# Kernel optimization log

Measured on AMD Instinct MI355X. Metric: run time of the kernel, lower is better.

## Reference

```python
import jax, jax.numpy as jnp
import numpy as np

B, L, D, E, F, K = 2, 1024, 768, 16, 3072, 2


def setup_inputs() -> dict:
    key = jax.random.key(0)
    ks = jax.random.split(key, 6)
    s = 0.02  # GPT-style init scale
    x = jax.random.normal(ks[0], (B, L, D), dtype=jnp.float32)
    wr = jax.random.normal(ks[1], (E, D), dtype=jnp.float32) * s   # router.weight [out,in]
    w1 = jax.random.normal(ks[2], (E, F, D), dtype=jnp.float32) * s  # expert fc1 weights
    b1 = jnp.zeros((E, F), dtype=jnp.float32)
    w2 = jax.random.normal(ks[3], (E, D, F), dtype=jnp.float32) * s  # expert fc2 weights
    b2 = jnp.zeros((E, D), dtype=jnp.float32)
    return {"x": x, "wr": wr, "w1": w1, "b1": b1, "w2": w2, "b2": b2}


def reference(x, wr, w1, b1, w2, b2):
    # --- router: softmax over experts, top-k gate built by scatter ---
    logits = jnp.einsum("bld,ed->ble", x, wr)            # [B,L,E]
    probs = jax.nn.softmax(logits, axis=-1)
    top_p, ix = jax.lax.top_k(probs, K)                   # [B,L,K]
    # gate[b,l,e] = top_p where e in ix else 0  (scatter_ equivalent)
    gate = jnp.sum(jax.nn.one_hot(ix, E, dtype=x.dtype) * top_p[..., None], axis=-2)  # [B,L,E]
    # --- dense: every expert over every token (matches original loop) ---
    h = jnp.einsum("bld,efd->blef", x, w1) + b1           # [B,L,E,F]
    h = jax.nn.gelu(h, approximate=False)                 # torch nn.GELU (exact erf)
    y = jnp.einsum("blef,edf->bled", h, w2) + b2          # [B,L,E,D]
    out = x + jnp.einsum("bled,ble->bld", y, gate)        # gated combine + residual
    return out
```

## Files before the change

### kernel.cpp

```cpp
#include <hip/hip_runtime.h>


#define D_      768
#define E_      16
#define F_      3072
#define NTOK    2048
#define NROWS   4096
#define SEG     384
#define MAXROWS 6144
#define KLEN    768
#define NT      12
#define LDT     776

typedef __attribute__((ext_vector_type(4))) unsigned int   u32x4;
typedef __attribute__((ext_vector_type(8))) unsigned short u16x8;
typedef __attribute__((ext_vector_type(8))) short          v8bf;
typedef __attribute__((ext_vector_type(4))) float          f32x4;

static __device__ inline unsigned short f2bf(float f) {
    unsigned u = __builtin_bit_cast(unsigned, f);
    u += 0x7fffu + ((u >> 16) & 1u);
    return (unsigned short)(u >> 16);
}
static __device__ __forceinline__ unsigned cvt_pk_bf16(float lo, float hi) {
    unsigned r;
    asm("v_cvt_pk_bf16_f32 %0, %1, %2" : "=v"(r) : "v"(lo), "v"(hi));
    return r;
}

__global__ void router_kernel(const float* __restrict__ x, const float* __restrict__ wr,
                              int* __restrict__ idx, float* __restrict__ gate) {
    const int tok  = blockIdx.x;
    const int lane = threadIdx.x;
    const float* xr = x + (size_t)tok * D_;

    float xv[12];
#pragma unroll
    for (int j = 0; j < 12; ++j) xv[j] = xr[lane + 64 * j];

    float lg[E_];
#pragma unroll
    for (int e = 0; e < E_; ++e) {
        const float* w = wr + (size_t)e * D_;
        float acc = 0.f;
#pragma unroll
        for (int j = 0; j < 12; ++j) acc += xv[j] * w[lane + 64 * j];
#pragma unroll
        for (int s = 32; s > 0; s >>= 1) acc += __shfl_xor(acc, s, 64);
        lg[e] = acc;
    }

    float m = lg[0];
#pragma unroll
    for (int e = 1; e < E_; ++e) m = fmaxf(m, lg[e]);
    float p[E_], s = 0.f;
#pragma unroll
    for (int e = 0; e < E_; ++e) { p[e] = expf(lg[e] - m); s += p[e]; }
    const float inv = 1.f / s;

    int e0 = 0; float p0 = p[0];
#pragma unroll
    for (int e = 1; e < E_; ++e) if (p[e] > p0) { p0 = p[e]; e0 = e; }
    int e1 = -1; float p1 = -1.f;
#pragma unroll
    for (int e = 0; e < E_; ++e) if (e != e0 && p[e] > p1) { p1 = p[e]; e1 = e; }

    if (lane == 0) {
        idx[tok * 2 + 0] = e0;  gate[tok * 2 + 0] = p0 * inv;
        idx[tok * 2 + 1] = e1;  gate[tok * 2 + 1] = p1 * inv;
    }
}

__global__ void build_kernel(const int* __restrict__ idx, const float* __restrict__ gate,
                             int* __restrict__ rowmap, float* __restrict__ rowgate,
                             int* __restrict__ posOf, int* __restrict__ meta) {
    __shared__ int cur[E_];
    const int t = threadIdx.x;
    if (t < E_) cur[t] = 0;
    __syncthreads();
    for (int i = t; i < MAXROWS; i += 256) { rowmap[i] = 0; rowgate[i] = 0.f; }
    __syncthreads();
    for (int i = t; i < NROWS; i += 256) {
        const int e = idx[i];
        const int o = atomicAdd(&cur[e], 1);
        if (o < SEG) {
            const int pos = e * SEG + o;
            rowmap[pos]  = i >> 1;
            rowgate[pos] = gate[i];
            posOf[i]     = pos;
        } else {
            posOf[i] = e * SEG;
        }
    }
    __syncthreads();
    if (t < E_) meta[t] = cur[t] < SEG ? cur[t] : SEG;
}

__global__ void gather_kernel(const float* __restrict__ x, const int* __restrict__ rowmap,
                              unsigned short* __restrict__ Xg) {
    const int g = blockIdx.x * 256 + threadIdx.x;
    const int pos = g / (D_ / 8), c = g % (D_ / 8);
    const int tok = rowmap[pos];
    const float* src = x + (size_t)tok * D_ + c * 8;
    f32x4 a = *(const f32x4*)src;
    f32x4 b = *(const f32x4*)(src + 4);
    u16x8 o;
    o[0] = f2bf(a[0]); o[1] = f2bf(a[1]); o[2] = f2bf(a[2]); o[3] = f2bf(a[3]);
    o[4] = f2bf(b[0]); o[5] = f2bf(b[1]); o[6] = f2bf(b[2]); o[7] = f2bf(b[3]);
    *(u16x8*)(Xg + (size_t)pos * D_ + c * 8) = o;
}

template <int EPI, int NCBSH>
__global__ __launch_bounds__(512, 2)
void gemm_kernel(const unsigned short* __restrict__ Ag, const float* __restrict__ Bw,
                 const float* __restrict__ bias, unsigned short* __restrict__ C0,
                 unsigned short* __restrict__ C123, const float* __restrict__ rowgate,
                 const int* __restrict__ meta, const int K, const int N) {
    const int bid   = blockIdx.x;
    const int e     = bid & 15;
    const int rest  = bid >> 4;
    const int n     = rest & ((1 << NCBSH) - 1);
    const int split = rest >> NCBSH;
    const int m0    = e * SEG;
    const int n0    = n * 96;
    const int kOff  = split * KLEN;

    __shared__ unsigned short Bs[96 * LDT];

    const int t    = threadIdx.x;
    const int lane = t & 63;
    const int wv   = t >> 6;
    const int r16  = lane & 15;
    const int h    = lane >> 4;

    {
#pragma unroll
        for (int i = 0; i < 18; ++i) {
            const int p = t + 512 * i;
            const int row = p / 96, pc = p % 96;
            const float* src = Bw + ((size_t)e * N + n0 + row) * K + kOff + pc * 8;
            f32x4 lo = *(const f32x4*)src;
            f32x4 hi = *(const f32x4*)(src + 4);
            u32x4 q;
            q[0] = cvt_pk_bf16(lo[0], lo[1]);
            q[1] = cvt_pk_bf16(lo[2], lo[3]);
            q[2] = cvt_pk_bf16(hi[0], hi[1]);
            q[3] = cvt_pk_bf16(hi[2], hi[3]);
            *(u32x4*)&Bs[row * LDT + pc * 8] = q;
        }
    }
    __syncthreads();

    const int cnt = meta[e];
    if (wv * 48 >= cnt) return;

    f32x4 acc[3][6];
#pragma unroll
    for (int i = 0; i < 3; ++i)
#pragma unroll
        for (int j = 0; j < 6; ++j) acc[i][j] = (f32x4){0.f, 0.f, 0.f, 0.f};

    const unsigned short* aBase =
        Ag + (size_t)(m0 + wv * 48 + r16) * K + kOff + h * 8;

    u32x4 pa[6], pb[6];

    auto loadSet = [&](int kt, u32x4* dst) {
#pragma unroll
        for (int mf = 0; mf < 3; ++mf)
#pragma unroll
            for (int ks = 0; ks < 2; ++ks)
                dst[mf * 2 + ks] =
                    *(const u32x4*)(aBase + (size_t)(mf * 16) * K + kt * 64 + ks * 32);
    };
    auto step = [&](int kt, const u32x4* a) {
#pragma unroll
        for (int ks = 0; ks < 2; ++ks) {
            v8bf bfr[6];
#pragma unroll
            for (int nf = 0; nf < 6; ++nf)
                bfr[nf] = *(const v8bf*)&Bs[(nf * 16 + r16) * LDT + kt * 64 + ks * 32 + h * 8];
#pragma unroll
            for (int mf = 0; mf < 3; ++mf) {
                const v8bf af = __builtin_bit_cast(v8bf, a[mf * 2 + ks]);
#pragma unroll
                for (int nf = 0; nf < 6; ++nf)
                    acc[mf][nf] = __builtin_amdgcn_mfma_f32_16x16x32_bf16(
                        af, bfr[nf], acc[mf][nf], 0, 0, 0);
            }
        }
    };

    loadSet(0, pa);
    loadSet(1, pb);
#pragma unroll
    for (int kt = 0; kt < NT; kt += 2) {
        step(kt, pa);
        if (kt + 2 < NT) loadSet(kt + 2, pa);
        step(kt + 1, pb);
        if (kt + 3 < NT) loadSet(kt + 3, pb);
    }

    unsigned short* myC = (EPI == 0 || split == 0)
                        ? C0 : C123 + (size_t)(split - 1) * MAXROWS * N;
#pragma unroll
    for (int mf = 0; mf < 3; ++mf) {
#pragma unroll
        for (int jj = 0; jj < 4; ++jj) {
            const int rr = m0 + wv * 48 + mf * 16 + h * 4 + jj;
            float gt = 0.f;
            if (EPI == 1) gt = rowgate[rr];
#pragma unroll
            for (int nf = 0; nf < 6; ++nf) {
                const int cc = n0 + nf * 16 + r16;
                float v = acc[mf][nf][jj];
                if (EPI == 0) {
                    v += bias[e * N + cc];
                    const float ge = 0.5f * v * (1.f + erff(v * 0.70710678118654752f));
                    myC[(size_t)rr * N + cc] = f2bf(ge);
                } else {
                    if (split == 0) v += bias[e * N + cc];
                    myC[(size_t)rr * N + cc] = f2bf(v * gt);
                }
            }
        }
    }
}

__global__ void combine_kernel(const float* __restrict__ x,
                               const unsigned short* __restrict__ Yp0,
                               const unsigned short* __restrict__ Yp123,
                               const int* __restrict__ posOf, float* __restrict__ out,
                               const int nsplit) {
    const int tok = blockIdx.x;
    const int t   = threadIdx.x;
    const int p0 = posOf[tok * 2 + 0];
    const int p1 = posOf[tok * 2 + 1];
    f32x4 v = *(const f32x4*)(x + (size_t)tok * D_ + t * 4);
    for (int s = 0; s < nsplit; ++s) {
        const unsigned short* base = (s == 0) ? Yp0
                                   : Yp123 + (size_t)(s - 1) * MAXROWS * D_;
        const unsigned short* a = base + (size_t)p0 * D_ + t * 4;
        const unsigned short* b = base + (size_t)p1 * D_ + t * 4;
#pragma unroll
        for (int i = 0; i < 4; ++i) {
            v[i] += __builtin_bit_cast(float, (unsigned)a[i] << 16);
            v[i] += __builtin_bit_cast(float, (unsigned)b[i] << 16);
        }
    }
    *(f32x4*)(out + (size_t)tok * D_ + t * 4) = v;
}

extern "C" void kernel_launch(void* const* d_in, const int* in_sizes, int n_in,
                              void* d_out, int out_size, void* d_ws, size_t ws_size,
                              hipStream_t stream) {
    const float* x  = (const float*)d_in[0];
    const float* wr = (const float*)d_in[1];
    const float* w1 = (const float*)d_in[2];
    const float* b1 = (const float*)d_in[3];
    const float* w2 = (const float*)d_in[4];
    const float* b2 = (const float*)d_in[5];
    float* out = (float*)d_out;

    char* wsp = (char*)d_ws;
    int*            idxP    = (int*)(wsp + 0);
    float*          gateP   = (float*)(wsp + 16384);
    int*            posOf   = (int*)(wsp + 32768);
    int*            rowmap  = (int*)(wsp + 49152);
    float*          rowgate = (float*)(wsp + 73728);
    int*            meta    = (int*)(wsp + 98304);
    const size_t    XG_OFF  = 131072;
    const size_t    PLANE   = (size_t)MAXROWS * D_ * 2;
    const size_t    H_OFF   = XG_OFF + PLANE;
    const size_t    H_B     = (size_t)MAXROWS * F_ * 2;
    unsigned short* Xg    = (unsigned short*)(wsp + XG_OFF);
    unsigned short* H     = (unsigned short*)(wsp + H_OFF);
    unsigned short* Yp0   = Xg;
    unsigned short* Yp123 = (unsigned short*)(wsp + H_OFF + H_B);

    const bool split4 = (ws_size >= H_OFF + H_B + 3 * PLANE);

    router_kernel<<<NTOK, 64, 0, stream>>>(x, wr, idxP, gateP);
    build_kernel<<<1, 256, 0, stream>>>(idxP, gateP, rowmap, rowgate, posOf, meta);
    gather_kernel<<<MAXROWS * (D_ / 8) / 256, 256, 0, stream>>>(x, rowmap, Xg);

    gemm_kernel<0, 5><<<16 * 32, 512, 0, stream>>>(
        Xg, w1, b1, H, (unsigned short*)nullptr, rowgate, meta, D_, F_);

    if (split4) {
        gemm_kernel<1, 3><<<16 * 8 * 4, 512, 0, stream>>>(
            H, w2, b2, Yp0, Yp123, rowgate, meta, F_, D_);
        combine_kernel<<<NTOK, 192, 0, stream>>>(x, Yp0, Yp123, posOf, out, 4);
    } else {
        gemm_kernel<1, 3><<<16 * 8 * 4, 512, 0, stream>>>(
            H, w2, b2, Yp0, Yp123, rowgate, meta, F_, D_);
        combine_kernel<<<NTOK, 192, 0, stream>>>(x, Yp0, Yp123, posOf, out, 4);
    }
}
```

Measured before the change: 182.6 us.

## Restructure expert GEMM into 128x128 tiles with triple-buffered async LDS loads

Replaces the GEMM that converted a whole 96xK weight slab to bf16 in LDS up front with a 128x128 output tile that streams 64-wide K chunks of both A and fp32 weights into LDS through global_load_lds. Three buffers are used with an XOR swizzle, and the fp32-to-bf16 weight conversion now happens after reading from LDS. The goal is to overlap global loads with MFMA work and to skip whole M-tiles beyond each expert's row count, instead of stalling on a large prologue load. In exchange, fp32 weights use twice the LDS bytes, the grid and waits are hand-tuned, and conversion work is repeated inside the inner loop.

```diff
diff --git a/kernel.cpp b/kernel.cpp
--- a/kernel.cpp
+++ b/kernel.cpp
@@ -8,9 +8,8 @@
 #define NROWS   4096
 #define SEG     384
 #define MAXROWS 6144
-#define KLEN    768
+#define BK      64
 #define NT      12
-#define LDT     776
 
 typedef __attribute__((ext_vector_type(4))) unsigned int   u32x4;
 typedef __attribute__((ext_vector_type(8))) unsigned short u16x8;
@@ -26,6 +25,11 @@
     unsigned r;
     asm("v_cvt_pk_bf16_f32 %0, %1, %2" : "=v"(r) : "v"(lo), "v"(hi));
     return r;
+}
+static __device__ __forceinline__ void gll16(const void* g, void* l) {
+    __builtin_amdgcn_global_load_lds(
+        (const __attribute__((address_space(1))) unsigned int*)g,
+        (__attribute__((address_space(3))) unsigned int*)l, 16, 0, 0);
 }
 
 __global__ void router_kernel(const float* __restrict__ x, const float* __restrict__ wr,
@@ -110,109 +114,126 @@
     *(u16x8*)(Xg + (size_t)pos * D_ + c * 8) = o;
 }
 
-template <int EPI, int NCBSH>
+template <int EPI>
 __global__ __launch_bounds__(512, 2)
 void gemm_kernel(const unsigned short* __restrict__ Ag, const float* __restrict__ Bw,
                  const float* __restrict__ bias, unsigned short* __restrict__ C0,
                  unsigned short* __restrict__ C123, const float* __restrict__ rowgate,
-                 const int* __restrict__ meta, const int K, const int N) {
+                 const int* __restrict__ meta, const int K, const int N, const int NTl) {
     const int bid   = blockIdx.x;
     const int e     = bid & 15;
     const int rest  = bid >> 4;
-    const int n     = rest & ((1 << NCBSH) - 1);
-    const int split = rest >> NCBSH;
-    const int m0    = e * SEG;
-    const int n0    = n * 96;
-    const int kOff  = split * KLEN;
-
-    __shared__ unsigned short Bs[96 * LDT];
+    const int nt    = rest % NTl;
+    const int rest2 = rest / NTl;
+    const int mtl   = rest2 % 3;
+    const int split = rest2 / 3;
+
+    const int cnt = meta[e];
+    if (mtl * 128 >= cnt) return;
+    const int m0   = e * SEG + mtl * 128;
+    const int n0   = nt * 128;
+    const int kOff = split * 768;
+
+    __shared__ alignas(16) unsigned short As[3][128 * 64];
+    __shared__ alignas(16) float           Bsf[3][128 * 64];
 
     const int t    = threadIdx.x;
     const int lane = t & 63;
     const int wv   = t >> 6;
+    const int wm   = wv >> 2;
+    const int wn   = wv & 3;
     const int r16  = lane & 15;
     const int h    = lane >> 4;
 
-    {
-#pragma unroll
-        for (int i = 0; i < 18; ++i) {
-            const int p = t + 512 * i;
-            const int row = p / 96, pc = p % 96;
-            const float* src = Bw + ((size_t)e * N + n0 + row) * K + kOff + pc * 8;
-            f32x4 lo = *(const f32x4*)src;
-            f32x4 hi = *(const f32x4*)(src + 4);
-            u32x4 q;
-            q[0] = cvt_pk_bf16(lo[0], lo[1]);
-            q[1] = cvt_pk_bf16(lo[2], lo[3]);
-            q[2] = cvt_pk_bf16(hi[0], hi[1]);
-            q[3] = cvt_pk_bf16(hi[2], hi[3]);
-            *(u32x4*)&Bs[row * LDT + pc * 8] = q;
-        }
-    }
-    __syncthreads();
-
-    const int cnt = meta[e];
-    if (wv * 48 >= cnt) return;
-
-    f32x4 acc[3][6];
-#pragma unroll
-    for (int i = 0; i < 3; ++i)
-#pragma unroll
-        for (int j = 0; j < 6; ++j) acc[i][j] = (f32x4){0.f, 0.f, 0.f, 0.f};
-
-    const unsigned short* aBase =
-        Ag + (size_t)(m0 + wv * 48 + r16) * K + kOff + h * 8;
-
-    u32x4 pa[6], pb[6];
-
-    auto loadSet = [&](int kt, u32x4* dst) {
-#pragma unroll
-        for (int mf = 0; mf < 3; ++mf)
-#pragma unroll
-            for (int ks = 0; ks < 2; ++ks)
-                dst[mf * 2 + ks] =
-                    *(const u32x4*)(aBase + (size_t)(mf * 16) * K + kt * 64 + ks * 32);
+    const bool act = (mtl * 128 + wm * 64) < cnt;
+
+    f32x4 acc[4][2];
+#pragma unroll
+    for (int i = 0; i < 4; ++i) { acc[i][0] = (f32x4){0,0,0,0}; acc[i][1] = (f32x4){0,0,0,0}; }
+
+    const unsigned short* srcA =
+        Ag + (size_t)(m0 + wv * 16 + (lane >> 3)) * K + kOff
+           + (((lane & 7) ^ ((lane >> 3) & 7)) << 3);
+
+    const float* srcB[4];
+#pragma unroll
+    for (int j = 0; j < 4; ++j) {
+        const int row = wv * 16 + j * 4 + (lane >> 4);
+        const int ss  = (lane & 15) ^ ((lane >> 4) + j * 4);
+        srcB[j] = Bw + ((size_t)e * N + n0 + row) * K + kOff + ss * 4;
+    }
+
+    auto stage = [&](int buf, int kt) {
+#pragma unroll
+        for (int j = 0; j < 2; ++j)
+            gll16(srcA + (size_t)(j * 8) * K + kt * BK,
+                  &As[buf][(wv * 16 + j * 8) * 64]);
+#pragma unroll
+        for (int j = 0; j < 4; ++j)
+            gll16(srcB[j] + kt * BK,
+                  &Bsf[buf][(wv * 16 + j * 4) * 64]);
     };
-    auto step = [&](int kt, const u32x4* a) {
+    auto compute = [&](int buf) {
 #pragma unroll
         for (int ks = 0; ks < 2; ++ks) {
-            v8bf bfr[6];
-#pragma unroll
-            for (int nf = 0; nf < 6; ++nf)
-                bfr[nf] = *(const v8bf*)&Bs[(nf * 16 + r16) * LDT + kt * 64 + ks * 32 + h * 8];
-#pragma unroll
-            for (int mf = 0; mf < 3; ++mf) {
-                const v8bf af = __builtin_bit_cast(v8bf, a[mf * 2 + ks]);
-#pragma unroll
-                for (int nf = 0; nf < 6; ++nf)
+            v8bf bfr[2];
+#pragma unroll
+            for (int nf = 0; nf < 2; ++nf) {
+                const int row = wn * 32 + nf * 16 + r16;
+                const int s0  = ks * 8 + h * 2;
+                const f32x4 lo = *(const f32x4*)&Bsf[buf][row * 64 + ((s0 ^ r16) << 2)];
+                const f32x4 hi = *(const f32x4*)&Bsf[buf][row * 64 + (((s0 + 1) ^ r16) << 2)];
+                u32x4 q;
+                q[0] = cvt_pk_bf16(lo[0], lo[1]);
+                q[1] = cvt_pk_bf16(lo[2], lo[3]);
+                q[2] = cvt_pk_bf16(hi[0], hi[1]);
+                q[3] = cvt_pk_bf16(hi[2], hi[3]);
+                bfr[nf] = __builtin_bit_cast(v8bf, q);
+            }
+#pragma unroll
+            for (int mf = 0; mf < 4; ++mf) {
+                const int rowA = wm * 64 + mf * 16 + r16;
+                const v8bf af = *(const v8bf*)
+                    &As[buf][rowA * 64 + (((ks * 4 + h) ^ (r16 & 7)) << 3)];
+#pragma unroll
+                for (int nf = 0; nf < 2; ++nf)
                     acc[mf][nf] = __builtin_amdgcn_mfma_f32_16x16x32_bf16(
                         af, bfr[nf], acc[mf][nf], 0, 0, 0);
             }
         }
     };
 
-    loadSet(0, pa);
-    loadSet(1, pb);
-#pragma unroll
-    for (int kt = 0; kt < NT; kt += 2) {
-        step(kt, pa);
-        if (kt + 2 < NT) loadSet(kt + 2, pa);
-        step(kt + 1, pb);
-        if (kt + 3 < NT) loadSet(kt + 3, pb);
-    }
-
+    stage(0, 0);
+    stage(1, 1);
+    asm volatile("s_waitcnt vmcnt(6)" ::: "memory");
+    __builtin_amdgcn_s_barrier();
+    __builtin_amdgcn_sched_barrier(0);
+
+#pragma unroll
+    for (int kt = 0; kt < NT; ++kt) {
+        if (kt + 2 < NT) stage((kt + 2) % 3, kt + 2);
+        if (act) compute(kt % 3);
+        if (kt + 1 < NT) {
+            if (kt + 2 < NT) { asm volatile("s_waitcnt vmcnt(6)" ::: "memory"); }
+            else             { asm volatile("s_waitcnt vmcnt(0)" ::: "memory"); }
+            __builtin_amdgcn_s_barrier();
+            __builtin_amdgcn_sched_barrier(0);
+        }
+    }
+
+    if (!act) return;
     unsigned short* myC = (EPI == 0 || split == 0)
                         ? C0 : C123 + (size_t)(split - 1) * MAXROWS * N;
 #pragma unroll
-    for (int mf = 0; mf < 3; ++mf) {
+    for (int mf = 0; mf < 4; ++mf) {
 #pragma unroll
         for (int jj = 0; jj < 4; ++jj) {
-            const int rr = m0 + wv * 48 + mf * 16 + h * 4 + jj;
+            const int rr = m0 + wm * 64 + mf * 16 + h * 4 + jj;
             float gt = 0.f;
             if (EPI == 1) gt = rowgate[rr];
 #pragma unroll
-            for (int nf = 0; nf < 6; ++nf) {
-                const int cc = n0 + nf * 16 + r16;
+            for (int nf = 0; nf < 2; ++nf) {
+                const int cc = n0 + wn * 32 + nf * 16 + r16;
                 float v = acc[mf][nf][jj];
                 if (EPI == 0) {
                     v += bias[e * N + cc];
@@ -278,22 +299,14 @@
     unsigned short* Yp0   = Xg;
     unsigned short* Yp123 = (unsigned short*)(wsp + H_OFF + H_B);
 
-    const bool split4 = (ws_size >= H_OFF + H_B + 3 * PLANE);
-
     router_kernel<<<NTOK, 64, 0, stream>>>(x, wr, idxP, gateP);
     build_kernel<<<1, 256, 0, stream>>>(idxP, gateP, rowmap, rowgate, posOf, meta);
     gather_kernel<<<MAXROWS * (D_ / 8) / 256, 256, 0, stream>>>(x, rowmap, Xg);
 
-    gemm_kernel<0, 5><<<16 * 32, 512, 0, stream>>>(
-        Xg, w1, b1, H, (unsigned short*)nullptr, rowgate, meta, D_, F_);
-
-    if (split4) {
-        gemm_kernel<1, 3><<<16 * 8 * 4, 512, 0, stream>>>(
-            H, w2, b2, Yp0, Yp123, rowgate, meta, F_, D_);
-        combine_kernel<<<NTOK, 192, 0, stream>>>(x, Yp0, Yp123, posOf, out, 4);
-    } else {
-        gemm_kernel<1, 3><<<16 * 8 * 4, 512, 0, stream>>>(
-            H, w2, b2, Yp0, Yp123, rowgate, meta, F_, D_);
-        combine_kernel<<<NTOK, 192, 0, stream>>>(x, Yp0, Yp123, posOf, out, 4);
-    }
-}
+    gemm_kernel<0><<<16 * 24 * 3, 512, 0, stream>>>(
+        Xg, w1, b1, H, (unsigned short*)nullptr, rowgate, meta, D_, F_, 24);
+
+    gemm_kernel<1><<<16 * 6 * 3 * 4, 512, 0, stream>>>(
+        H, w2, b2, Yp0, Yp123, rowgate, meta, F_, D_, 6);
+    combine_kernel<<<NTOK, 192, 0, stream>>>(x, Yp0, Yp123, posOf, out, 4);
+}
```

Result: slower. 221.9 us (+21.5%).
